# Performance work log

Hardware: AMD Instinct MI355X
Metric: run time of the kernel (lower is better)

## Reference

```python
import jax, jax.numpy as jnp
import numpy as np

BATCH = 65536
IN_FEATURES = 128
OUT_FEATURES = 128
GRID = 8  # initial_grid: number of RBF/spline basis centers per edge


def setup_inputs() -> dict:
    key = jax.random.key(0)
    k1, k2, k3 = jax.random.split(key, 3)
    x = jax.random.normal(k1, (BATCH, IN_FEATURES), dtype=jnp.float32)
    # Per-edge spline coefficients stacked: [out, in, grid]
    coeffs = jax.random.normal(k2, (OUT_FEATURES, IN_FEATURES, GRID), dtype=jnp.float32) * 0.1
    # Per-edge base (SiLU) weights stacked: [out, in]
    base_w = jax.random.normal(k3, (OUT_FEATURES, IN_FEATURES), dtype=jnp.float32) * 0.1
    # Shared uniform grid of RBF centers in [-1, 1]
    centers = jnp.linspace(-1.0, 1.0, GRID, dtype=jnp.float32)
    return {"x": x, "coeffs": coeffs, "base_w": base_w, "centers": centers}


def reference(x, coeffs, base_w, centers):
    # HybridBasisFunction per edge: base_w * silu(x) + sum_g coeffs[g] * exp(-((x-c_g)/w)^2)
    width = 2.0 / (GRID - 1)  # grid spacing
    # basis: [B, in, G]
    diff = (x[:, :, None] - centers[None, None, :]) / width
    basis = jnp.exp(-diff * diff)
    # Sum over all edges (j -> i): output[b, i] = sum_j phi_ij(x[b, j])
    out = jnp.einsum('big,oig->bo', basis, coeffs)
    out = out + jnp.einsum('bi,oi->bo', jax.nn.silu(x), base_w)
    return out
```

## Files before the change

### kernel.cpp

```cpp
#include <hip/hip_runtime.h>

typedef __fp16       pk16x2 __attribute__((ext_vector_type(2)));
typedef _Float16     f16x8  __attribute__((ext_vector_type(8)));
typedef float        f32x4  __attribute__((ext_vector_type(4)));
typedef float        f32x16 __attribute__((ext_vector_type(16)));
typedef unsigned int u32x4  __attribute__((ext_vector_type(4)));

#define BATCH 65536
#define NIN   128
#define NOUT  128

#define L2E   1.4426950408889634f
#define SQL2E 1.2011224087864498f
#define EM2   0.1353352832366127f


__global__ __launch_bounds__(256) void kan_prep(const float* __restrict__ coeffs,
                                                const float* __restrict__ base_w,
                                                _Float16* __restrict__ W3) {
    int t = blockIdx.x * 256 + threadIdx.x;
    int ks   = t >> 8;
    int c    = t & 255;
    int nbb  = c >> 6;
    int lane = c & 63;
    int sub  = lane >> 5;
    int col  = nbb * 32 + (lane & 31);
    f16x8 v;
    if (ks < 64) {
        int g = ks >> 3, t2 = ks & 7;
        const float* src = coeffs + ((size_t)col * 128 + g * 16 + sub * 8 + t2) * 8;
#pragma unroll
        for (int e = 0; e < 8; ++e) v[e] = (_Float16)src[e];
    } else {
        const float* src = base_w + (size_t)col * 128 + (ks - 64) * 16 + sub * 8;
#pragma unroll
        for (int e = 0; e < 8; ++e) v[e] = (_Float16)src[e];
    }
    *(f16x8*)((char*)W3 + (size_t)t * 16) = v;
}

__device__ __forceinline__ void gll16(const void* g, void* l) {
    __builtin_amdgcn_global_load_lds(
        (const __attribute__((address_space(1))) unsigned int*)g,
        (__attribute__((address_space(3))) unsigned int*)l, 16, 0, 0);
}

__device__ __forceinline__ f16x8 basis8r(float t) {
    float u  = t * SQL2E;
    float b0 = __builtin_amdgcn_exp2f(-(u * u));
    float r  = __builtin_amdgcn_exp2f(__builtin_fmaf(t, 2.0f * L2E, -L2E));
    float b1 = b0 * r; r *= EM2;
    float b2 = b1 * r; r *= EM2;
    float b3 = b2 * r; r *= EM2;
    float b4 = b3 * r; r *= EM2;
    float b5 = b4 * r; r *= EM2;
    float b6 = b5 * r; r *= EM2;
    float b7 = b6 * r;
    u32x4 U;
    U[0] = __builtin_bit_cast(unsigned int, __builtin_amdgcn_cvt_pkrtz(b0, b1));
    U[1] = __builtin_bit_cast(unsigned int, __builtin_amdgcn_cvt_pkrtz(b2, b3));
    U[2] = __builtin_bit_cast(unsigned int, __builtin_amdgcn_cvt_pkrtz(b4, b5));
    U[3] = __builtin_bit_cast(unsigned int, __builtin_amdgcn_cvt_pkrtz(b6, b7));
    return __builtin_bit_cast(f16x8, U);
}

__device__ __forceinline__ float silu1(float xv) {
    float p = __builtin_amdgcn_exp2f(-xv * L2E);
    return xv * __builtin_amdgcn_rcpf(1.0f + p);
}

__global__ __launch_bounds__(256, 2) void kan_main(const float* __restrict__ x,
                                                   const _Float16* __restrict__ W3,
                                                   float* __restrict__ out) {
    __shared__ _Float16 smem[2][16384];

    const int tid   = threadIdx.x;
    const int lane  = tid & 63;
    const int w     = tid >> 6;
    const int l31   = lane & 31;
    const int sub   = lane >> 5;
    const int row0  = blockIdx.x * 128 + w * 32;
    const int start = blockIdx.x & 7;

    const int slp = (blockIdx.x & 1) + ((blockIdx.x >> 8) & 1);
    if (slp > 0) __builtin_amdgcn_s_sleep(10);
    if (slp > 1) __builtin_amdgcn_s_sleep(10);

    const float* xp = x + (size_t)(row0 + l31) * NIN;

    f32x16 acc[4];
#pragma unroll
    for (int nbb = 0; nbb < 4; ++nbb)
#pragma unroll
        for (int r = 0; r < 16; ++r) acc[nbb][r] = 0.f;

    const char* wbase = (const char*)W3;
#define STAGE(buf, grp)                                                         \
    do {                                                                        \
        const char* _s = wbase + (size_t)(grp) * 32768 + (size_t)tid * 16;      \
        char*       _d = (char*)&smem[(buf)][0] + (size_t)tid * 16;             \
        _Pragma("unroll")                                                       \
        for (int _i = 0; _i < 8; ++_i) gll16(_s + _i * 4096, _d + _i * 4096);   \
    } while (0)

    STAGE(0, start);
    f32x4 xa = *(const f32x4*)(xp + start * 16 + sub * 8);
    f32x4 xb = *(const f32x4*)(xp + start * 16 + sub * 8 + 4);
    __syncthreads();

#pragma unroll
    for (int i = 0; i < 8; ++i) {
        const int cur  = i & 1;
        const int nxtg = (i < 7) ? ((start + i + 1) & 7) : 8;
        STAGE(cur ^ 1, nxtg);
        const int nxt = (i < 7) ? (((start + i + 1) & 7) * 16) : 0;
        f32x4 xa2 = *(const f32x4*)(xp + nxt + sub * 8);
        f32x4 xb2 = *(const f32x4*)(xp + nxt + sub * 8 + 4);

        const char* bpbase = (const char*)&smem[cur][0] + lane * 16;

        f16x8 a[8];
        a[0] = basis8r(__builtin_fmaf(xa[0], 3.5f, 3.5f));
        a[1] = basis8r(__builtin_fmaf(xa[1], 3.5f, 3.5f));
        f16x8 b[4];
#pragma unroll
        for (int q = 0; q < 4; ++q) b[q] = *(const f16x8*)(bpbase + q * 1024);

#pragma unroll
        for (int t2 = 0; t2 < 8; ++t2) {
            f16x8 bn[4];
            if (t2 < 7) {
#pragma unroll
                for (int q = 0; q < 4; ++q)
                    bn[q] = *(const f16x8*)(bpbase + (t2 + 1) * 4096 + q * 1024);
            }
            if (t2 < 6) {
                float xs = (t2 + 2 < 4) ? xa[t2 + 2] : xb[(t2 + 2) & 3];
                a[t2 + 2] = basis8r(__builtin_fmaf(xs, 3.5f, 3.5f));
            }
#pragma unroll
            for (int q = 0; q < 4; ++q)
                acc[q] = __builtin_amdgcn_mfma_f32_32x32x16_f16(a[t2], b[q], acc[q], 0, 0, 0);
            if (t2 < 7) {
#pragma unroll
                for (int q = 0; q < 4; ++q) b[q] = bn[q];
            }
        }
        xa = xa2; xb = xb2;
        __syncthreads();
    }

#pragma unroll
    for (int s = 0; s < 8; ++s) {
        f32x4 xa2, xb2;
        if (s < 7) {
            xa2 = *(const f32x4*)(xp + (s + 1) * 16 + sub * 8);
            xb2 = *(const f32x4*)(xp + (s + 1) * 16 + sub * 8 + 4);
        }
        u32x4 U;
        U[0] = __builtin_bit_cast(unsigned int,
               __builtin_amdgcn_cvt_pkrtz(silu1(xa[0]), silu1(xa[1])));
        U[1] = __builtin_bit_cast(unsigned int,
               __builtin_amdgcn_cvt_pkrtz(silu1(xa[2]), silu1(xa[3])));
        U[2] = __builtin_bit_cast(unsigned int,
               __builtin_amdgcn_cvt_pkrtz(silu1(xb[0]), silu1(xb[1])));
        U[3] = __builtin_bit_cast(unsigned int,
               __builtin_amdgcn_cvt_pkrtz(silu1(xb[2]), silu1(xb[3])));
        f16x8 a = __builtin_bit_cast(f16x8, U);
        const char* bp = (const char*)&smem[0][0] + s * 4096 + lane * 16;
#pragma unroll
        for (int q = 0; q < 4; ++q) {
            f16x8 bq = *(const f16x8*)(bp + q * 1024);
            acc[q] = __builtin_amdgcn_mfma_f32_32x32x16_f16(a, bq, acc[q], 0, 0, 0);
        }
        if (s < 7) { xa = xa2; xb = xb2; }
    }

#pragma unroll
    for (int q = 0; q < 4; ++q)
#pragma unroll
        for (int r = 0; r < 16; ++r) {
            int crow = (r & 3) + 8 * (r >> 2) + 4 * sub;
            out[(size_t)(row0 + crow) * NOUT + q * 32 + l31] = acc[q][r];
        }
}

extern "C" void kernel_launch(void* const* d_in, const int* in_sizes, int n_in,
                              void* d_out, int out_size, void* d_ws, size_t ws_size,
                              hipStream_t stream) {
    const float* x       = (const float*)d_in[0];
    const float* coeffs  = (const float*)d_in[1];
    const float* base_w  = (const float*)d_in[2];
    _Float16* W3 = (_Float16*)d_ws;

    kan_prep<<<dim3(72), dim3(256), 0, stream>>>(coeffs, base_w, W3);
    kan_main<<<dim3(BATCH / 128), dim3(256), 0, stream>>>(x, W3, (float*)d_out);
}
```

Before: 39.87 us.

## Split MFMA accumulators into two chains and drop staggered start and sleeps

Uses two independent accumulator sets (accA/accB) so consecutive MFMAs alternate between chains, which shortens the dependency stalls between back-to-back MFMA ops on the same accumulator. All eight basis vectors are computed up front rather than interleaved with the MFMAs, and B fragments are loaded directly without explicit register double-buffering. It also removes the per-block rotated group start and the s_sleep staggering, so all blocks now walk the weight groups in the same order. Doubling the accumulators to 128 VGPRs per thread adds register pressure, which may limit occupancy at two blocks per CU, and the removed staggering may bring back contention on the shared weight reads.

```diff
diff --git a/kernel.cpp b/kernel.cpp
--- a/kernel.cpp
+++ b/kernel.cpp
@@ -74,25 +74,20 @@
                                                    float* __restrict__ out) {
     __shared__ _Float16 smem[2][16384];
 
-    const int tid   = threadIdx.x;
-    const int lane  = tid & 63;
-    const int w     = tid >> 6;
-    const int l31   = lane & 31;
-    const int sub   = lane >> 5;
-    const int row0  = blockIdx.x * 128 + w * 32;
-    const int start = blockIdx.x & 7;
-
-    const int slp = (blockIdx.x & 1) + ((blockIdx.x >> 8) & 1);
-    if (slp > 0) __builtin_amdgcn_s_sleep(10);
-    if (slp > 1) __builtin_amdgcn_s_sleep(10);
+    const int tid  = threadIdx.x;
+    const int lane = tid & 63;
+    const int w    = tid >> 6;
+    const int l31  = lane & 31;
+    const int sub  = lane >> 5;
+    const int row0 = blockIdx.x * 128 + w * 32;
 
     const float* xp = x + (size_t)(row0 + l31) * NIN;
 
-    f32x16 acc[4];
+    f32x16 accA[4], accB[4];
 #pragma unroll
-    for (int nbb = 0; nbb < 4; ++nbb)
+    for (int q = 0; q < 4; ++q)
 #pragma unroll
-        for (int r = 0; r < 16; ++r) acc[nbb][r] = 0.f;
+        for (int r = 0; r < 16; ++r) { accA[q][r] = 0.f; accB[q][r] = 0.f; }
 
     const char* wbase = (const char*)W3;
 #define STAGE(buf, grp)                                                         \
@@ -103,47 +98,38 @@
         for (int _i = 0; _i < 8; ++_i) gll16(_s + _i * 4096, _d + _i * 4096);   \
     } while (0)
 
-    STAGE(0, start);
-    f32x4 xa = *(const f32x4*)(xp + start * 16 + sub * 8);
-    f32x4 xb = *(const f32x4*)(xp + start * 16 + sub * 8 + 4);
+    STAGE(0, 0);
+    f32x4 xa = *(const f32x4*)(xp + sub * 8);
+    f32x4 xb = *(const f32x4*)(xp + sub * 8 + 4);
     __syncthreads();
 
 #pragma unroll
-    for (int i = 0; i < 8; ++i) {
-        const int cur  = i & 1;
-        const int nxtg = (i < 7) ? ((start + i + 1) & 7) : 8;
-        STAGE(cur ^ 1, nxtg);
-        const int nxt = (i < 7) ? (((start + i + 1) & 7) * 16) : 0;
+    for (int g = 0; g < 8; ++g) {
+        const int cur = g & 1;
+        STAGE(cur ^ 1, g + 1);
+        const int nxt = (g < 7) ? (g + 1) * 16 : 0;
         f32x4 xa2 = *(const f32x4*)(xp + nxt + sub * 8);
         f32x4 xb2 = *(const f32x4*)(xp + nxt + sub * 8 + 4);
 
-        const char* bpbase = (const char*)&smem[cur][0] + lane * 16;
-
         f16x8 a[8];
-        a[0] = basis8r(__builtin_fmaf(xa[0], 3.5f, 3.5f));
-        a[1] = basis8r(__builtin_fmaf(xa[1], 3.5f, 3.5f));
-        f16x8 b[4];
 #pragma unroll
-        for (int q = 0; q < 4; ++q) b[q] = *(const f16x8*)(bpbase + q * 1024);
+        for (int t2 = 0; t2 < 4; ++t2) a[t2]     = basis8r(__builtin_fmaf(xa[t2], 3.5f, 3.5f));
+#pragma unroll
+        for (int t2 = 0; t2 < 4; ++t2) a[4 + t2] = basis8r(__builtin_fmaf(xb[t2], 3.5f, 3.5f));
 
 #pragma unroll
-        for (int t2 = 0; t2 < 8; ++t2) {
-            f16x8 bn[4];
-            if (t2 < 7) {
+        for (int tp = 0; tp < 4; ++tp) {
+            const char* bpa = (const char*)&smem[cur][0] + (tp * 2) * 4096 + lane * 16;
+            const char* bpb = bpa + 4096;
 #pragma unroll
-                for (int q = 0; q < 4; ++q)
-                    bn[q] = *(const f16x8*)(bpbase + (t2 + 1) * 4096 + q * 1024);
-            }
-            if (t2 < 6) {
-                float xs = (t2 + 2 < 4) ? xa[t2 + 2] : xb[(t2 + 2) & 3];
-                a[t2 + 2] = basis8r(__builtin_fmaf(xs, 3.5f, 3.5f));
+            for (int q = 0; q < 4; ++q) {
+                f16x8 b = *(const f16x8*)(bpa + q * 1024);
+                accA[q] = __builtin_amdgcn_mfma_f32_32x32x16_f16(a[tp * 2], b, accA[q], 0, 0, 0);
             }
 #pragma unroll
-            for (int q = 0; q < 4; ++q)
-                acc[q] = __builtin_amdgcn_mfma_f32_32x32x16_f16(a[t2], b[q], acc[q], 0, 0, 0);
-            if (t2 < 7) {
-#pragma unroll
-                for (int q = 0; q < 4; ++q) b[q] = bn[q];
+            for (int q = 0; q < 4; ++q) {
+                f16x8 b = *(const f16x8*)(bpb + q * 1024);
+                accB[q] = __builtin_amdgcn_mfma_f32_32x32x16_f16(a[tp * 2 + 1], b, accB[q], 0, 0, 0);
             }
         }
         xa = xa2; xb = xb2;
@@ -151,29 +137,41 @@
     }
 
 #pragma unroll
-    for (int s = 0; s < 8; ++s) {
-        f32x4 xa2, xb2;
-        if (s < 7) {
-            xa2 = *(const f32x4*)(xp + (s + 1) * 16 + sub * 8);
-            xb2 = *(const f32x4*)(xp + (s + 1) * 16 + sub * 8 + 4);
+    for (int sp = 0; sp < 4; ++sp) {
+#pragma unroll
+        for (int half = 0; half < 2; ++half) {
+            const int s = sp * 2 + half;
+            f32x4 xa2, xb2;
+            if (s < 7) {
+                xa2 = *(const f32x4*)(xp + (s + 1) * 16 + sub * 8);
+                xb2 = *(const f32x4*)(xp + (s + 1) * 16 + sub * 8 + 4);
+            }
+            u32x4 U;
+            U[0] = __builtin_bit_cast(unsigned int,
+                   __builtin_amdgcn_cvt_pkrtz(silu1(xa[0]), silu1(xa[1])));
+            U[1] = __builtin_bit_cast(unsigned int,
+                   __builtin_amdgcn_cvt_pkrtz(silu1(xa[2]), silu1(xa[3])));
+            U[2] = __builtin_bit_cast(unsigned int,
+                   __builtin_amdgcn_cvt_pkrtz(silu1(xb[0]), silu1(xb[1])));
+            U[3] = __builtin_bit_cast(unsigned int,
+                   __builtin_amdgcn_cvt_pkrtz(silu1(xb[2]), silu1(xb[3])));
+            f16x8 a = __builtin_bit_cast(f16x8, U);
+            const char* bp = (const char*)&smem[0][0] + s * 4096 + lane * 16;
+            if (half == 0) {
+#pragma unroll
+                for (int q = 0; q < 4; ++q) {
+                    f16x8 bq = *(const f16x8*)(bp + q * 1024);
+                    accA[q] = __builtin_amdgcn_mfma_f32_32x32x16_f16(a, bq, accA[q], 0, 0, 0);
+                }
+            } else {
+#pragma unroll
+                for (int q = 0; q < 4; ++q) {
+                    f16x8 bq = *(const f16x8*)(bp + q * 1024);
+                    accB[q] = __builtin_amdgcn_mfma_f32_32x32x16_f16(a, bq, accB[q], 0, 0, 0);
+                }
+            }
+            if (s < 7) { xa = xa2; xb = xb2; }
         }
-        u32x4 U;
-        U[0] = __builtin_bit_cast(unsigned int,
-               __builtin_amdgcn_cvt_pkrtz(silu1(xa[0]), silu1(xa[1])));
-        U[1] = __builtin_bit_cast(unsigned int,
-               __builtin_amdgcn_cvt_pkrtz(silu1(xa[2]), silu1(xa[3])));
-        U[2] = __builtin_bit_cast(unsigned int,
-               __builtin_amdgcn_cvt_pkrtz(silu1(xb[0]), silu1(xb[1])));
-        U[3] = __builtin_bit_cast(unsigned int,
-               __builtin_amdgcn_cvt_pkrtz(silu1(xb[2]), silu1(xb[3])));
-        f16x8 a = __builtin_bit_cast(f16x8, U);
-        const char* bp = (const char*)&smem[0][0] + s * 4096 + lane * 16;
-#pragma unroll
-        for (int q = 0; q < 4; ++q) {
-            f16x8 bq = *(const f16x8*)(bp + q * 1024);
-            acc[q] = __builtin_amdgcn_mfma_f32_32x32x16_f16(a, bq, acc[q], 0, 0, 0);
-        }
-        if (s < 7) { xa = xa2; xb = xb2; }
     }
 
 #pragma unroll
@@ -181,7 +179,7 @@
 #pragma unroll
         for (int r = 0; r < 16; ++r) {
             int crow = (r & 3) + 8 * (r >> 2) + 4 * sub;
-            out[(size_t)(row0 + crow) * NOUT + q * 32 + l31] = acc[q][r];
+            out[(size_t)(row0 + crow) * NOUT + q * 32 + l31] = accA[q][r] + accB[q][r];
         }
 }
 
```

Result: faster. 38.34 us (-3.8%).
